# Kernel optimization log

Measured on AMD Instinct MI355X. Metric: run time of the kernel, lower is better.

The kernel has to match this reference:

```python
import jax, jax.numpy as jnp
import numpy as np

N = 20000      # nodes
E = 320000     # edges
S = 256        # scalar (0e) channels of irreps_feature
F = 960        # full irreps_feature dim (256x0e+128x1e+64x2e)
NB = 32        # number_of_basis
CUT = 5.0      # max_radius


def setup_inputs() -> dict:
    key = jax.random.key(0)
    ks = jax.random.split(key, 24)
    def w(k, shape):
        return jax.random.normal(k, shape, jnp.float32) / np.sqrt(shape[0])
    return {
        "node_feature": jax.random.normal(ks[0], (N, F), jnp.float32),
        "pos": jax.random.normal(ks[1], (N, 3), jnp.float32),
        "edge_index": jax.random.randint(ks[2], (2, E), 0, N),
        "W_ai1": w(ks[3], (S, S)), "b_ai1": jnp.zeros((S,), jnp.float32),
        "W_ai2": w(ks[4], (S, 1)), "b_ai2": jnp.zeros((1,), jnp.float32),
        "W_ci1": w(ks[5], (S, S)), "b_ci1": jnp.zeros((S,), jnp.float32),
        "W_ci2": w(ks[6], (S, 1)), "b_ci2": jnp.zeros((1,), jnp.float32),
        "W_sc": w(ks[7], (S, S)), "b_sc": jnp.zeros((S,), jnp.float32),
        "W_ed": w(ks[8], (NB, S)), "b_ed": jnp.zeros((S,), jnp.float32),
        "W_b1": w(ks[9], (3 * S, S)), "b_b1": jnp.zeros((S,), jnp.float32),
        "W_b2": w(ks[10], (S, 1)), "b_b2": jnp.zeros((1,), jnp.float32),
    }


def _rbf(d):
    # ExpNormalSmearing (torchmd-net), cutoff_lower=0, cutoff_upper=CUT, non-trainable
    start = np.exp(-CUT)
    means = jnp.linspace(start, 1.0, NB, dtype=jnp.float32)
    beta = jnp.float32(((2.0 / NB) * (1.0 - start)) ** -2)
    cosine_cut = 0.5 * (jnp.cos(np.pi * d / CUT) + 1.0) * (d < CUT)
    return cosine_cut[:, None] * jnp.exp(-beta * (jnp.exp(-d)[:, None] - means) ** 2)


def reference(node_feature, pos, edge_index,
              W_ai1, b_ai1, W_ai2, b_ai2,
              W_ci1, b_ci1, W_ci2, b_ci2,
              W_sc, b_sc, W_ed, b_ed,
              W_b1, b_b1, W_b2, b_b2):
    # LinearRS(irreps_feature -> 0e) only touches the 0e block (first S channels)
    scal = node_feature[:, :S]
    silu = jax.nn.silu

    log_ai = silu(scal @ W_ai1 + b_ai1) @ W_ai2 + b_ai2          # [N,1]
    ai = jnp.exp(log_ai)
    log_ci = silu(scal @ W_ci1 + b_ci1) @ W_ci2 + b_ci2          # [N,1]
    ci = jnp.exp(log_ci)

    src, dst = edge_index[0], edge_index[1]
    rel = pos[dst] - pos[src]                                     # [E,3]
    norm = jnp.linalg.norm(rel, axis=1, keepdims=True)            # [E,1]
    rhat = rel / (norm + 1e-8)
    emb = _rbf(norm[:, 0])                                        # [E,NB]

    node_sc = scal @ W_sc + b_sc                                  # project once, gather [N,S]
    src_f = node_sc[src]
    dst_f = node_sc[dst]
    edge_f = emb @ W_ed + b_ed
    edge_feature = jnp.concatenate([src_f, dst_f, edge_f], axis=-1)  # [E,3S]
    bij = silu(edge_feature @ W_b1 + b_b1) @ W_b2 + b_b2          # [E,1]

    # edge softmax over incoming edges of dst, with extra ci mass
    bmax = jax.ops.segment_max(bij, dst, num_segments=N)
    bmax = jnp.where(jnp.isneginf(bmax), 0.0, bmax)
    bij_exp = jnp.exp(bij - bmax[dst])
    bsum = jax.ops.segment_sum(bij_exp, dst, num_segments=N) + ci  # [N,1]
    gamma = bij_exp / (bsum[dst] + 1e-7)                           # [E,1]

    bij_prime = gamma * ai[dst]                                    # [E,1]
    outer = rhat[:, :, None] * rhat[:, None, :]                    # [E,3,3]
    contrib = jax.ops.segment_sum(bij_prime[:, :, None] * outer, dst, num_segments=N)  # [N,3,3]

    eye3 = jnp.eye(3, dtype=pos.dtype)
    sigma = ai[:, :, None] * eye3 - contrib + 1e-6 * eye3          # [N,3,3]
    sum_gamma = jax.ops.segment_sum(gamma, dst, num_segments=N)    # [N,1]
    return sigma, ai, sum_gamma
```

## Files before the change

kernel.cpp:

```cpp
#include <hip/hip_runtime.h>
#include <math.h>

#define N_NODES 20000
#define E_EDGES 320000
#define F_DIM   960
#define S_DIM   256
#define QTAB    2048
#define ASTRIDE 264
#define CAP     64

typedef __attribute__((ext_vector_type(8))) short short8;
typedef __attribute__((ext_vector_type(4))) float f32x4;
typedef _Float16 half8 __attribute__((ext_vector_type(8)));

__device__ __forceinline__ float siluf(float x) {
    return x / (1.0f + __expf(-x));
}

__device__ __forceinline__ unsigned short bf16rn(float x) {
    unsigned u = __float_as_uint(x);
    return (unsigned short)((u + 0x7FFFu + ((u >> 16) & 1u)) >> 16);
}

__global__ void prep_kernel(const float* __restrict__ W_sc, const float* __restrict__ W_ed,
                            const float* __restrict__ W_b1, const float* __restrict__ b_sc,
                            const float* __restrict__ b_ed, const float* __restrict__ b_b1,
                            const float* __restrict__ W_ai1, const float* __restrict__ W_ci1,
                            float* __restrict__ Bcat, float* __restrict__ We, float* __restrict__ c0,
                            int* __restrict__ cnt)
{
    int idx = blockIdx.x * 256 + threadIdx.x;
    if (idx < N_NODES) cnt[idx] = 0;
    if (idx < 256 * 1024) {
        int k = idx >> 10, j = idx & 1023;
        float s = 0.0f;
        if (j < 256) {
            for (int m = 0; m < 256; ++m) s += W_sc[k * 256 + m] * W_b1[m * 256 + j];
        } else if (j < 512) {
            int jj = j - 256;
            for (int m = 0; m < 256; ++m) s += W_sc[k * 256 + m] * W_b1[(256 + m) * 256 + jj];
        } else if (j < 768) {
            s = W_ai1[k * 256 + (j - 512)];
        } else {
            s = W_ci1[k * 256 + (j - 768)];
        }
        Bcat[idx] = s;
    } else if (idx < 256 * 1024 + 32 * 256) {
        int t = idx - 256 * 1024;
        int p = t >> 8, j = t & 255;
        float s = 0.0f;
        for (int m = 0; m < 256; ++m) s += W_ed[p * 256 + m] * W_b1[(512 + m) * 256 + j];
        We[t] = s;
    } else if (idx < 256 * 1024 + 32 * 256 + 256) {
        int j = idx - 256 * 1024 - 32 * 256;
        float s = b_b1[j];
        for (int m = 0; m < 256; ++m) {
            s += b_sc[m] * (W_b1[m * 256 + j] + W_b1[(256 + m) * 256 + j]);
            s += b_ed[m] * W_b1[(512 + m) * 256 + j];
        }
        c0[j] = s;
    }
}

__global__ void aux_kernel(const int* __restrict__ ei, int* __restrict__ cnt, int* __restrict__ rank,
                           const float* __restrict__ Bcat, unsigned short* __restrict__ Bpack,
                           const float* __restrict__ We, _Float16* __restrict__ Tab,
                           const float* __restrict__ nf, unsigned short* __restrict__ scalp)
{
    int b = blockIdx.x;
    if (b < 1250) {
        int i = b * 256 + threadIdx.x;
        rank[i] = atomicAdd(&cnt[ei[E_EDGES + i]], 1);
    } else if (b < 1378) {
        int idx = (b - 1250) * 256 + threadIdx.x;
        int kq = idx & 3, j = (idx >> 2) & 1023, t = idx >> 12;
        #pragma unroll
        for (int jj = 0; jj < 8; ++jj)
            Bpack[idx * 8 + jj] = bf16rn(Bcat[(t * 32 + kq * 8 + jj) * 1024 + j]);
    } else if (b < 3426) {
        int idx = (b - 1378) * 256 + threadIdx.x;
        int q = idx >> 8, j = idx & 255;
        float nrm = 5.0f * (float)q / (float)(QTAB - 1);
        const float start = 0.006737946999085467f;
        const float mustep = (1.0f - start) / 31.0f;
        const float bx = (2.0f / 32.0f) * (1.0f - start);
        const float beta = 1.0f / (bx * bx);
        const float PI_F = 3.14159265358979323846f;
        float cc = (nrm < 5.0f) ? 0.5f * (__cosf(PI_F * nrm * 0.2f) + 1.0f) : 0.0f;
        float t = __expf(-nrm);
        float s = 0.0f;
        for (int k = 0; k < 32; ++k) {
            float dm = t - (start + (float)k * mustep);
            s += __expf(-beta * dm * dm) * We[k * 256 + j];
        }
        Tab[idx] = (_Float16)(cc * s);
    } else {
        int idx = (b - 3426) * 256 + threadIdx.x;
        int base = idx * 4;
        int n = base >> 8, k = base & 255;
        float4 a4 = *(const float4*)&nf[(size_t)n * F_DIM + k];
        ushort4 b4;
        b4.x = bf16rn(a4.x); b4.y = bf16rn(a4.y);
        b4.z = bf16rn(a4.z); b4.w = bf16rn(a4.w);
        *(ushort4*)&scalp[n * 256 + k] = b4;
    }
}

__global__ __launch_bounds__(1024) void scan_kernel(const int* __restrict__ cnt,
                                                    int* __restrict__ start)
{
    extern __shared__ int ls[];
    __shared__ int ps[1024];
    const int t = threadIdx.x;
    for (int i = t; i < N_NODES; i += 1024) ls[i] = cnt[i];
    __syncthreads();

    const int base = t * 20;
    int loc[20];
    int s = 0;
    #pragma unroll
    for (int i = 0; i < 20; ++i) {
        int n = (base + i < N_NODES) ? ls[base + i] : 0;
        loc[i] = s; s += n;
    }
    ps[t] = s;
    __syncthreads();
    for (int off = 1; off < 1024; off <<= 1) {
        int v = (t >= off) ? ps[t - off] : 0;
        __syncthreads();
        ps[t] += v;
        __syncthreads();
    }
    int offset = ps[t] - s;
    #pragma unroll
    for (int i = 0; i < 20; ++i)
        if (base + i < N_NODES) ls[base + i] = offset + loc[i];
    __syncthreads();
    for (int i = t; i < N_NODES; i += 1024) start[i] = ls[i];
}

__global__ void edge_geom_kernel(const int* __restrict__ ei, const int* __restrict__ start,
                                 const int* __restrict__ rank, const float* __restrict__ pos,
                                 int2* __restrict__ sd, float4* __restrict__ geom)
{
    int i = blockIdx.x * 256 + threadIdx.x;
    if (i >= E_EDGES) return;
    int s = ei[i];
    int d = ei[E_EDGES + i];
    int slot = start[d] + rank[i];
    int2 p; p.x = s; p.y = d;
    sd[slot] = p;

    float px = pos[3 * d + 0] - pos[3 * s + 0];
    float py = pos[3 * d + 1] - pos[3 * s + 1];
    float pz = pos[3 * d + 2] - pos[3 * s + 2];
    float nrm = sqrtf(px * px + py * py + pz * pz);
    float inv = 1.0f / (nrm + 1e-8f);
    float4 o;
    o.x = px * inv; o.y = py * inv; o.z = pz * inv;
    o.w = nrm * (float)(QTAB - 1) * 0.2f;
    geom[slot] = o;
}

__global__ __launch_bounds__(256) void node_mfma_kernel(
    const unsigned short* __restrict__ scalp, const unsigned short* __restrict__ Bpack,
    const float* __restrict__ c0,
    const float* __restrict__ b_ai1, const float* __restrict__ W_ai2, const float* __restrict__ b_ai2,
    const float* __restrict__ b_ci1, const float* __restrict__ W_ci2, const float* __restrict__ b_ci2,
    _Float16* __restrict__ u, _Float16* __restrict__ v,
    float* __restrict__ bsumseed, float* __restrict__ out_ai)
{
    __shared__ unsigned short A[32 * ASTRIDE];
    __shared__ float red[32 * 4];

    const int tid = threadIdx.x;
    const int w = tid >> 6, lane = tid & 63;
    const int bg = blockIdx.x & 1;
    const int m0 = (blockIdx.x >> 1) * 32;
    const int col16 = lane & 15, quad = lane >> 4;

    #pragma unroll
    for (int it = 0; it < 4; ++it) {
        int idx = (it * 256 + tid) * 8;
        int r = idx >> 8, c = idx & 255;
        *(uint4*)&A[r * ASTRIDE + c] = *(const uint4*)&scalp[(m0 + r) * 256 + c];
    }
    __syncthreads();

    for (int cc = 0; cc < 2; ++cc) {
        const int cg = bg * 2 + cc;
        f32x4 acc[2][4];
        #pragma unroll
        for (int mt = 0; mt < 2; ++mt)
            #pragma unroll
            for (int nt = 0; nt < 4; ++nt)
                acc[mt][nt] = (f32x4){0.0f, 0.0f, 0.0f, 0.0f};

        const int colbase = cg * 256 + w * 64;

        for (int t = 0; t < 8; ++t) {
            short8 af[2];
            #pragma unroll
            for (int mt = 0; mt < 2; ++mt)
                af[mt] = *(const short8*)&A[(mt * 16 + col16) * ASTRIDE + t * 32 + quad * 8];
            short8 bf[4];
            #pragma unroll
            for (int nt = 0; nt < 4; ++nt)
                bf[nt] = *(const short8*)&Bpack[(((t * 1024 + colbase + nt * 16 + col16) * 4) + quad) * 8];
            #pragma unroll
            for (int mt = 0; mt < 2; ++mt)
                #pragma unroll
                for (int nt = 0; nt < 4; ++nt)
                    acc[mt][nt] = __builtin_amdgcn_mfma_f32_16x16x32_bf16(af[mt], bf[nt], acc[mt][nt], 0, 0, 0);
        }

        if (cg == 0) {
            #pragma unroll
            for (int nt = 0; nt < 4; ++nt) {
                int jl = w * 64 + nt * 16 + col16;
                float c0v = c0[jl];
                #pragma unroll
                for (int mt = 0; mt < 2; ++mt)
                    #pragma unroll
                    for (int reg = 0; reg < 4; ++reg)
                        u[(m0 + mt * 16 + quad * 4 + reg) * 256 + jl] = (_Float16)(acc[mt][nt][reg] + c0v);
        }
        } else if (cg == 1) {
            #pragma unroll
            for (int nt = 0; nt < 4; ++nt) {
                int jl = w * 64 + nt * 16 + col16;
                #pragma unroll
                for (int mt = 0; mt < 2; ++mt)
                    #pragma unroll
                    for (int reg = 0; reg < 4; ++reg)
                        v[(m0 + mt * 16 + quad * 4 + reg) * 256 + jl] = (_Float16)(acc[mt][nt][reg]);
            }
        } else {
            const float* b1 = (cg == 2) ? b_ai1 : b_ci1;
            const float* w2 = (cg == 2) ? W_ai2 : W_ci2;
            float s[2][4] = {{0, 0, 0, 0}, {0, 0, 0, 0}};
            #pragma unroll
            for (int nt = 0; nt < 4; ++nt) {
                int jl = w * 64 + nt * 16 + col16;
                float bb = b1[jl], ww = w2[jl];
                #pragma unroll
                for (int mt = 0; mt < 2; ++mt)
                    #pragma unroll
                    for (int reg = 0; reg < 4; ++reg)
                        s[mt][reg] += siluf(acc[mt][nt][reg] + bb) * ww;
            }
            #pragma unroll
            for (int off = 1; off < 16; off <<= 1) {
                #pragma unroll
                for (int mt = 0; mt < 2; ++mt)
                    #pragma unroll
                    for (int reg = 0; reg < 4; ++reg)
                        s[mt][reg] += __shfl_xor(s[mt][reg], off);
            }
            if (col16 == 0) {
                #pragma unroll
                for (int mt = 0; mt < 2; ++mt)
                    #pragma unroll
                    for (int reg = 0; reg < 4; ++reg)
                        red[(mt * 16 + quad * 4 + reg) * 4 + w] = s[mt][reg];
            }
            __syncthreads();
            if (tid < 32) {
                float sum = red[tid * 4] + red[tid * 4 + 1] + red[tid * 4 + 2] + red[tid * 4 + 3];
                if (cg == 2) out_ai[m0 + tid] = expf(sum + b_ai2[0]);
                else         bsumseed[m0 + tid] = expf(sum + b_ci2[0]) + 1e-7f;
            }
            __syncthreads();
        }
    }
}

__global__ __launch_bounds__(256) void edge_bij_kernel(
    const int2* __restrict__ sd, const float4* __restrict__ geom,
    const _Float16* __restrict__ u, const _Float16* __restrict__ v,
    const _Float16* __restrict__ Tab,
    const float* __restrict__ W_b2, const float* __restrict__ b_b2,
    float* __restrict__ bijV)
{
    const int l = threadIdx.x & 15;
    const int slot = blockIdx.x * 16 + (threadIdx.x >> 4);
    const int2 e = sd[slot];
    const int src = e.x;
    const int dst = e.y;
    const float x = ((const float*)&geom[slot])[3];

    int qi = (int)x;
    float f = x - (float)qi;
    if (qi >= QTAB - 1) { qi = QTAB - 2; f = 1.0f; }
    const _Float16 fh = (_Float16)f;

    float w2c[16];
    #pragma unroll
    for (int c = 0; c < 16; c += 4)
        *(float4*)&w2c[c] = *(const float4*)&W_b2[l * 16 + c];

    const unsigned lo = (unsigned)l * 32u;
    const char* ub = (const char*)u + ((unsigned)src * 512u + lo);
    const char* vb = (const char*)v + ((unsigned)dst * 512u + lo);
    const char* tb = (const char*)Tab + ((unsigned)qi * 512u + lo);

    half8 u0 = *(const half8*)(ub);
    half8 u1 = *(const half8*)(ub + 16);
    half8 v0 = *(const half8*)(vb);
    half8 v1 = *(const half8*)(vb + 16);
    half8 t00 = *(const half8*)(tb);
    half8 t01 = *(const half8*)(tb + 16);
    half8 t10 = *(const half8*)(tb + 512);
    half8 t11 = *(const half8*)(tb + 528);

    half8 h0 = (u0 + v0) + (t00 + fh * (t10 - t00));
    half8 h1 = (u1 + v1) + (t01 + fh * (t11 - t01));

    float acc = 0.0f;
    #pragma unroll
    for (int c = 0; c < 8; ++c) {
        float hf = (float)h0[c];
        float sig = __builtin_amdgcn_rcpf(1.0f + __expf(-hf));
        acc += w2c[c] * hf * sig;
    }
    #pragma unroll
    for (int c = 0; c < 8; ++c) {
        float hf = (float)h1[c];
        float sig = __builtin_amdgcn_rcpf(1.0f + __expf(-hf));
        acc += w2c[8 + c] * hf * sig;
    }
    #pragma unroll
    for (int off = 1; off < 16; off <<= 1) acc += __shfl_xor(acc, off);

    if (l == 0) bijV[slot] = acc + b_b2[0];
}

__global__ __launch_bounds__(256) void node_reduce_kernel(
    const int* __restrict__ start, const int* __restrict__ cnt,
    const float* __restrict__ bijV, const float4* __restrict__ geom,
    const float* __restrict__ bsumseed, const float* __restrict__ out_ai,
    float* __restrict__ out_sigma, float* __restrict__ out_sg)
{
    const int grp = threadIdx.x >> 4;
    const int l = threadIdx.x & 15;
    const int g = blockIdx.x * 16 + grp;
    const int st = start[g];
    const int deg = min(cnt[g], CAP);

    float bj[4], ex[4], ey[4], ez[4];
    bool ok[4];
    float m = -1e30f;
    #pragma unroll
    for (int k = 0; k < 4; ++k) {
        int i = l + k * 16;
        ok[k] = (i < deg);
        if (ok[k]) {
            float4 o = geom[st + i];
            bj[k] = bijV[st + i];
            ex[k] = o.x; ey[k] = o.y; ez[k] = o.z;
        } else {
            bj[k] = -1e30f; ex[k] = 0.0f; ey[k] = 0.0f; ez[k] = 0.0f;
        }
        m = fmaxf(m, bj[k]);
    }
    #pragma unroll
    for (int off = 1; off < 16; off <<= 1) m = fmaxf(m, __shfl_xor(m, off));

    float g4[4];
    float ssum = 0.0f;
    #pragma unroll
    for (int k = 0; k < 4; ++k) {
        g4[k] = ok[k] ? __expf(bj[k] - m) : 0.0f;
        ssum += g4[k];
    }
    #pragma unroll
    for (int off = 1; off < 16; off <<= 1) ssum += __shfl_xor(ssum, off);

    float invt = 1.0f / (ssum + bsumseed[g]);

    float a0 = 0, a1 = 0, a2 = 0, a3 = 0, a4 = 0, a5 = 0, a6 = 0;
    #pragma unroll
    for (int k = 0; k < 4; ++k) {
        float gm = g4[k] * invt;
        a0 += gm * ex[k] * ex[k]; a1 += gm * ey[k] * ey[k]; a2 += gm * ez[k] * ez[k];
        a3 += gm * ex[k] * ey[k]; a4 += gm * ex[k] * ez[k]; a5 += gm * ey[k] * ez[k];
        a6 += gm;
    }
    #pragma unroll
    for (int off = 1; off < 16; off <<= 1) {
        a0 += __shfl_xor(a0, off); a1 += __shfl_xor(a1, off);
        a2 += __shfl_xor(a2, off); a3 += __shfl_xor(a3, off);
        a4 += __shfl_xor(a4, off); a5 += __shfl_xor(a5, off);
        a6 += __shfl_xor(a6, off);
    }

    if (l == 0) {
        float ai = out_ai[g];
        float* sg = &out_sigma[g * 9];
        float d0 = ai + 1e-6f;
        sg[0] = d0 - ai * a0;
        sg[1] = -ai * a3;
        sg[2] = -ai * a4;
        sg[3] = -ai * a3;
        sg[4] = d0 - ai * a1;
        sg[5] = -ai * a5;
        sg[6] = -ai * a4;
        sg[7] = -ai * a5;
        sg[8] = d0 - ai * a2;
        out_sg[g] = a6;
    }
}

extern "C" void kernel_launch(void* const* d_in, const int* in_sizes, int n_in,
                              void* d_out, int out_size, void* d_ws, size_t ws_size,
                              hipStream_t stream)
{
    const float* nf    = (const float*)d_in[0];
    const float* pos   = (const float*)d_in[1];
    const int*   ei    = (const int*)  d_in[2];
    const float* W_ai1 = (const float*)d_in[3];
    const float* b_ai1 = (const float*)d_in[4];
    const float* W_ai2 = (const float*)d_in[5];
    const float* b_ai2 = (const float*)d_in[6];
    const float* W_ci1 = (const float*)d_in[7];
    const float* b_ci1 = (const float*)d_in[8];
    const float* W_ci2 = (const float*)d_in[9];
    const float* b_ci2 = (const float*)d_in[10];
    const float* W_sc  = (const float*)d_in[11];
    const float* b_sc  = (const float*)d_in[12];
    const float* W_ed  = (const float*)d_in[13];
    const float* b_ed  = (const float*)d_in[14];
    const float* W_b1  = (const float*)d_in[15];
    const float* b_b1  = (const float*)d_in[16];
    const float* W_b2  = (const float*)d_in[17];
    const float* b_b2  = (const float*)d_in[18];

    char* pb = (char*)d_ws;
    auto alloc = [&](size_t bytes) -> void* {
        void* r = (void*)pb;
        pb += (bytes + 255) & ~(size_t)255;
        return r;
    };
    float*          Bcat    = (float*)         alloc(262144 * 4);
    float*          We      = (float*)         alloc(8192 * 4);
    float*          c0      = (float*)         alloc(256 * 4);
    _Float16*       Tab     = (_Float16*)      alloc((size_t)QTAB * 256 * 2);
    unsigned short* Bpack   = (unsigned short*)alloc((size_t)256 * 1024 * 2);
    unsigned short* scalp   = (unsigned short*)alloc((size_t)N_NODES * 256 * 2);
    _Float16*       u       = (_Float16*)      alloc((size_t)N_NODES * 256 * 2);
    _Float16*       v       = (_Float16*)      alloc((size_t)N_NODES * 256 * 2);
    float*          bsumseed= (float*)         alloc((size_t)N_NODES * 4);
    int*            cnt     = (int*)           alloc((size_t)N_NODES * 4);
    int*            startA  = (int*)           alloc((size_t)N_NODES * 4);
    int*            rank    = (int*)           alloc((size_t)E_EDGES * 4);
    int2*           sd      = (int2*)          alloc((size_t)E_EDGES * 8);
    float4*         geom    = (float4*)        alloc((size_t)E_EDGES * 16);
    float*          bijV    = (float*)         alloc((size_t)E_EDGES * 4);

    float* out       = (float*)d_out;
    float* out_sigma = out;
    float* out_ai    = out + N_NODES * 9;
    float* out_sg    = out + N_NODES * 10;

    prep_kernel<<<1058, 256, 0, stream>>>(W_sc, W_ed, W_b1, b_sc, b_ed, b_b1, W_ai1, W_ci1,
                                          Bcat, We, c0, cnt);
    aux_kernel<<<8426, 256, 0, stream>>>(ei, cnt, rank, Bcat, Bpack, We, Tab, nf, scalp);
    scan_kernel<<<1, 1024, (size_t)N_NODES * 4, stream>>>(cnt, startA);
    edge_geom_kernel<<<1250, 256, 0, stream>>>(ei, startA, rank, pos, sd, geom);
    node_mfma_kernel<<<1250, 256, 0, stream>>>(scalp, Bpack, c0, b_ai1, W_ai2, b_ai2,
                                               b_ci1, W_ci2, b_ci2, u, v, bsumseed, out_ai);
    edge_bij_kernel<<<20000, 256, 0, stream>>>(sd, geom, u, v, Tab, W_b2, b_b2, bijV);
    node_reduce_kernel<<<1250, 256, 0, stream>>>(startA, cnt, bijV, geom, bsumseed, out_ai,
                                                 out_sigma, out_sg);
}
```

Measured before the change: 286.5 us.

## Fuse weight packing into prep, merge scan into node MFMA kernel

The prep kernel now computes eight folded-weight rows per thread and writes bf16-packed MFMA operands directly. This removes the fp32 Bcat buffer and its separate repack pass. The single-block prefix scan becomes an extra block of the node MFMA kernel, so it no longer needs its own serial launch. The MFMA tiles are enlarged to 64 rows with one column group per block. In exchange, accumulator register pressure rises and the scan runs with fewer threads doing longer serial loops.

```diff
diff --git a/kernel.cpp b/kernel.cpp
--- a/kernel.cpp
+++ b/kernel.cpp
@@ -22,48 +22,72 @@
     return (unsigned short)((u + 0x7FFFu + ((u >> 16) & 1u)) >> 16);
 }
 
-__global__ void prep_kernel(const float* __restrict__ W_sc, const float* __restrict__ W_ed,
-                            const float* __restrict__ W_b1, const float* __restrict__ b_sc,
-                            const float* __restrict__ b_ed, const float* __restrict__ b_b1,
-                            const float* __restrict__ W_ai1, const float* __restrict__ W_ci1,
-                            float* __restrict__ Bcat, float* __restrict__ We, float* __restrict__ c0,
-                            int* __restrict__ cnt)
-{
-    int idx = blockIdx.x * 256 + threadIdx.x;
-    if (idx < N_NODES) cnt[idx] = 0;
-    if (idx < 256 * 1024) {
-        int k = idx >> 10, j = idx & 1023;
-        float s = 0.0f;
+__global__ __launch_bounds__(256) void prep_kernel(
+    const float* __restrict__ W_sc, const float* __restrict__ W_ed,
+    const float* __restrict__ W_b1, const float* __restrict__ b_sc,
+    const float* __restrict__ b_ed, const float* __restrict__ b_b1,
+    const float* __restrict__ W_ai1, const float* __restrict__ W_ci1,
+    unsigned short* __restrict__ Bpack, float* __restrict__ We, float* __restrict__ c0,
+    int* __restrict__ cnt)
+{
+    const int b = blockIdx.x;
+    const int tid = threadIdx.x;
+    if (b < 128) {
+        const int oct = b >> 2;
+        const int j   = (b & 3) * 256 + tid;
+        const int k0  = oct * 8;
+        float s[8];
+        #pragma unroll
+        for (int jj = 0; jj < 8; ++jj) s[jj] = 0.0f;
         if (j < 256) {
-            for (int m = 0; m < 256; ++m) s += W_sc[k * 256 + m] * W_b1[m * 256 + j];
+            for (int m = 0; m < 256; ++m) {
+                float wv = W_b1[m * 256 + j];
+                #pragma unroll
+                for (int jj = 0; jj < 8; ++jj) s[jj] += W_sc[(k0 + jj) * 256 + m] * wv;
+            }
         } else if (j < 512) {
-            int jj = j - 256;
-            for (int m = 0; m < 256; ++m) s += W_sc[k * 256 + m] * W_b1[(256 + m) * 256 + jj];
+            const int j2 = j - 256;
+            for (int m = 0; m < 256; ++m) {
+                float wv = W_b1[(256 + m) * 256 + j2];
+                #pragma unroll
+                for (int jj = 0; jj < 8; ++jj) s[jj] += W_sc[(k0 + jj) * 256 + m] * wv;
+            }
         } else if (j < 768) {
-            s = W_ai1[k * 256 + (j - 512)];
+            #pragma unroll
+            for (int jj = 0; jj < 8; ++jj) s[jj] = W_ai1[(k0 + jj) * 256 + (j - 512)];
         } else {
-            s = W_ci1[k * 256 + (j - 768)];
-        }
-        Bcat[idx] = s;
-    } else if (idx < 256 * 1024 + 32 * 256) {
-        int t = idx - 256 * 1024;
-        int p = t >> 8, j = t & 255;
+            #pragma unroll
+            for (int jj = 0; jj < 8; ++jj) s[jj] = W_ci1[(k0 + jj) * 256 + (j - 768)];
+        }
+        unsigned short o[8];
+        #pragma unroll
+        for (int jj = 0; jj < 8; ++jj) o[jj] = bf16rn(s[jj]);
+        unsigned short* dst = &Bpack[((oct >> 2) * 4096 + j * 4 + (oct & 3)) * 8];
+        ushort4 lo; lo.x = o[0]; lo.y = o[1]; lo.z = o[2]; lo.w = o[3];
+        ushort4 hi; hi.x = o[4]; hi.y = o[5]; hi.z = o[6]; hi.w = o[7];
+        *(ushort4*)dst = lo;
+        *(ushort4*)(dst + 4) = hi;
+    } else if (b < 160) {
+        const int t = (b - 128) * 256 + tid;
+        const int p = t >> 8, j = t & 255;
         float s = 0.0f;
         for (int m = 0; m < 256; ++m) s += W_ed[p * 256 + m] * W_b1[(512 + m) * 256 + j];
         We[t] = s;
-    } else if (idx < 256 * 1024 + 32 * 256 + 256) {
-        int j = idx - 256 * 1024 - 32 * 256;
+    } else if (b == 160) {
+        const int j = tid;
         float s = b_b1[j];
         for (int m = 0; m < 256; ++m) {
             s += b_sc[m] * (W_b1[m * 256 + j] + W_b1[(256 + m) * 256 + j]);
             s += b_ed[m] * W_b1[(512 + m) * 256 + j];
         }
         c0[j] = s;
+    } else {
+        const int idx = (b - 161) * 256 + tid;
+        if (idx < N_NODES) cnt[idx] = 0;
     }
 }
 
 __global__ void aux_kernel(const int* __restrict__ ei, int* __restrict__ cnt, int* __restrict__ rank,
-                           const float* __restrict__ Bcat, unsigned short* __restrict__ Bpack,
                            const float* __restrict__ We, _Float16* __restrict__ Tab,
                            const float* __restrict__ nf, unsigned short* __restrict__ scalp)
 {
@@ -71,14 +95,8 @@
     if (b < 1250) {
         int i = b * 256 + threadIdx.x;
         rank[i] = atomicAdd(&cnt[ei[E_EDGES + i]], 1);
-    } else if (b < 1378) {
+    } else if (b < 3298) {
         int idx = (b - 1250) * 256 + threadIdx.x;
-        int kq = idx & 3, j = (idx >> 2) & 1023, t = idx >> 12;
-        #pragma unroll
-        for (int jj = 0; jj < 8; ++jj)
-            Bpack[idx * 8 + jj] = bf16rn(Bcat[(t * 32 + kq * 8 + jj) * 1024 + j]);
-    } else if (b < 3426) {
-        int idx = (b - 1378) * 256 + threadIdx.x;
         int q = idx >> 8, j = idx & 255;
         float nrm = 5.0f * (float)q / (float)(QTAB - 1);
         const float start = 0.006737946999085467f;
@@ -95,7 +113,7 @@
         }
         Tab[idx] = (_Float16)(cc * s);
     } else {
-        int idx = (b - 3426) * 256 + threadIdx.x;
+        int idx = (b - 3298) * 256 + threadIdx.x;
         int base = idx * 4;
         int n = base >> 8, k = base & 255;
         float4 a4 = *(const float4*)&nf[(size_t)n * F_DIM + k];
@@ -106,37 +124,149 @@
     }
 }
 
-__global__ __launch_bounds__(1024) void scan_kernel(const int* __restrict__ cnt,
-                                                    int* __restrict__ start)
-{
-    extern __shared__ int ls[];
-    __shared__ int ps[1024];
-    const int t = threadIdx.x;
-    for (int i = t; i < N_NODES; i += 1024) ls[i] = cnt[i];
+__global__ __launch_bounds__(256) void mfma_scan_kernel(
+    const unsigned short* __restrict__ scalp, const unsigned short* __restrict__ Bpack,
+    const float* __restrict__ c0,
+    const float* __restrict__ b_ai1, const float* __restrict__ W_ai2, const float* __restrict__ b_ai2,
+    const float* __restrict__ b_ci1, const float* __restrict__ W_ci2, const float* __restrict__ b_ci2,
+    _Float16* __restrict__ u, _Float16* __restrict__ v,
+    float* __restrict__ bsumseed, float* __restrict__ out_ai,
+    const int* __restrict__ cnt, int* __restrict__ startA)
+{
+    __shared__ unsigned short A[64 * ASTRIDE];
+    __shared__ float red[64 * 4];
+
+    const int tid = threadIdx.x;
+
+    if (blockIdx.x == 1252) {
+        int* ps = (int*)A;
+        const int base = tid * 79;
+        int ssum = 0;
+        for (int i = 0; i < 79; ++i) {
+            int idx = base + i;
+            ssum += (idx < N_NODES) ? cnt[idx] : 0;
+        }
+        ps[tid] = ssum;
+        __syncthreads();
+        for (int off = 1; off < 256; off <<= 1) {
+            int vv = (tid >= off) ? ps[tid - off] : 0;
+            __syncthreads();
+            ps[tid] += vv;
+            __syncthreads();
+        }
+        int run = ps[tid] - ssum;
+        for (int i = 0; i < 79; ++i) {
+            int idx = base + i;
+            if (idx < N_NODES) { int c = cnt[idx]; startA[idx] = run; run += c; }
+        }
+        return;
+    }
+
+    const int w = tid >> 6, lane = tid & 63;
+    const int cg = blockIdx.x & 3;
+    const int m0 = (blockIdx.x >> 2) * 64;
+    const int col16 = lane & 15, quad = lane >> 4;
+
+    #pragma unroll
+    for (int it = 0; it < 8; ++it) {
+        int idx = (it * 256 + tid) * 8;
+        int r = idx >> 8, c = idx & 255;
+        *(uint4*)&A[r * ASTRIDE + c] = *(const uint4*)&scalp[(size_t)(m0 + r) * 256 + c];
+    }
     __syncthreads();
 
-    const int base = t * 20;
-    int loc[20];
-    int s = 0;
-    #pragma unroll
-    for (int i = 0; i < 20; ++i) {
-        int n = (base + i < N_NODES) ? ls[base + i] : 0;
-        loc[i] = s; s += n;
-    }
-    ps[t] = s;
-    __syncthreads();
-    for (int off = 1; off < 1024; off <<= 1) {
-        int v = (t >= off) ? ps[t - off] : 0;
+    f32x4 acc[4][4];
+    #pragma unroll
+    for (int mt = 0; mt < 4; ++mt)
+        #pragma unroll
+        for (int nt = 0; nt < 4; ++nt)
+            acc[mt][nt] = (f32x4){0.0f, 0.0f, 0.0f, 0.0f};
+
+    const int colbase = cg * 256 + w * 64;
+
+    for (int t = 0; t < 8; ++t) {
+        short8 af[4];
+        #pragma unroll
+        for (int mt = 0; mt < 4; ++mt)
+            af[mt] = *(const short8*)&A[(mt * 16 + col16) * ASTRIDE + t * 32 + quad * 8];
+        short8 bf[4];
+        #pragma unroll
+        for (int nt = 0; nt < 4; ++nt)
+            bf[nt] = *(const short8*)&Bpack[(((t * 1024 + colbase + nt * 16 + col16) * 4) + quad) * 8];
+        #pragma unroll
+        for (int mt = 0; mt < 4; ++mt)
+            #pragma unroll
+            for (int nt = 0; nt < 4; ++nt)
+                acc[mt][nt] = __builtin_amdgcn_mfma_f32_16x16x32_bf16(af[mt], bf[nt], acc[mt][nt], 0, 0, 0);
+    }
+
+    if (cg == 0) {
+        #pragma unroll
+        for (int nt = 0; nt < 4; ++nt) {
+            int jl = w * 64 + nt * 16 + col16;
+            float c0v = c0[jl];
+            #pragma unroll
+            for (int mt = 0; mt < 4; ++mt)
+                #pragma unroll
+                for (int reg = 0; reg < 4; ++reg) {
+                    int row = m0 + mt * 16 + quad * 4 + reg;
+                    if (row < N_NODES)
+                        u[(size_t)row * 256 + jl] = (_Float16)(acc[mt][nt][reg] + c0v);
+                }
+        }
+    } else if (cg == 1) {
+        #pragma unroll
+        for (int nt = 0; nt < 4; ++nt) {
+            int jl = w * 64 + nt * 16 + col16;
+            #pragma unroll
+            for (int mt = 0; mt < 4; ++mt)
+                #pragma unroll
+                for (int reg = 0; reg < 4; ++reg) {
+                    int row = m0 + mt * 16 + quad * 4 + reg;
+                    if (row < N_NODES)
+                        v[(size_t)row * 256 + jl] = (_Float16)(acc[mt][nt][reg]);
+                }
+        }
+    } else {
+        const float* b1 = (cg == 2) ? b_ai1 : b_ci1;
+        const float* w2 = (cg == 2) ? W_ai2 : W_ci2;
+        float s[4][4];
+        #pragma unroll
+        for (int mt = 0; mt < 4; ++mt)
+            #pragma unroll
+            for (int reg = 0; reg < 4; ++reg) s[mt][reg] = 0.0f;
+        #pragma unroll
+        for (int nt = 0; nt < 4; ++nt) {
+            int jl = w * 64 + nt * 16 + col16;
+            float bb = b1[jl], ww = w2[jl];
+            #pragma unroll
+            for (int mt = 0; mt < 4; ++mt)
+                #pragma unroll
+                for (int reg = 0; reg < 4; ++reg)
+                    s[mt][reg] += siluf(acc[mt][nt][reg] + bb) * ww;
+        }
+        #pragma unroll
+        for (int off = 1; off < 16; off <<= 1) {
+            #pragma unroll
+            for (int mt = 0; mt < 4; ++mt)
+                #pragma unroll
+                for (int reg = 0; reg < 4; ++reg)
+                    s[mt][reg] += __shfl_xor(s[mt][reg], off);
+        }
+        if (col16 == 0) {
+            #pragma unroll
+            for (int mt = 0; mt < 4; ++mt)
+                #pragma unroll
+                for (int reg = 0; reg < 4; ++reg)
+                    red[(mt * 16 + quad * 4 + reg) * 4 + w] = s[mt][reg];
+        }
         __syncthreads();
-        ps[t] += v;
-        __syncthreads();
-    }
-    int offset = ps[t] - s;
-    #pragma unroll
-    for (int i = 0; i < 20; ++i)
-        if (base + i < N_NODES) ls[base + i] = offset + loc[i];
-    __syncthreads();
-    for (int i = t; i < N_NODES; i += 1024) start[i] = ls[i];
+        if (tid < 64 && m0 + tid < N_NODES) {
+            float sum = red[tid * 4] + red[tid * 4 + 1] + red[tid * 4 + 2] + red[tid * 4 + 3];
+            if (cg == 2) out_ai[m0 + tid] = expf(sum + b_ai2[0]);
+            else         bsumseed[m0 + tid] = expf(sum + b_ci2[0]) + 1e-7f;
+        }
+    }
 }
 
 __global__ void edge_geom_kernel(const int* __restrict__ ei, const int* __restrict__ start,
@@ -160,119 +290,6 @@
     o.x = px * inv; o.y = py * inv; o.z = pz * inv;
     o.w = nrm * (float)(QTAB - 1) * 0.2f;
     geom[slot] = o;
-}
-
-__global__ __launch_bounds__(256) void node_mfma_kernel(
-    const unsigned short* __restrict__ scalp, const unsigned short* __restrict__ Bpack,
-    const float* __restrict__ c0,
-    const float* __restrict__ b_ai1, const float* __restrict__ W_ai2, const float* __restrict__ b_ai2,
-    const float* __restrict__ b_ci1, const float* __restrict__ W_ci2, const float* __restrict__ b_ci2,
-    _Float16* __restrict__ u, _Float16* __restrict__ v,
-    float* __restrict__ bsumseed, float* __restrict__ out_ai)
-{
-    __shared__ unsigned short A[32 * ASTRIDE];
-    __shared__ float red[32 * 4];
-
-    const int tid = threadIdx.x;
-    const int w = tid >> 6, lane = tid & 63;
-    const int bg = blockIdx.x & 1;
-    const int m0 = (blockIdx.x >> 1) * 32;
-    const int col16 = lane & 15, quad = lane >> 4;
-
-    #pragma unroll
-    for (int it = 0; it < 4; ++it) {
-        int idx = (it * 256 + tid) * 8;
-        int r = idx >> 8, c = idx & 255;
-        *(uint4*)&A[r * ASTRIDE + c] = *(const uint4*)&scalp[(m0 + r) * 256 + c];
-    }
-    __syncthreads();
-
-    for (int cc = 0; cc < 2; ++cc) {
-        const int cg = bg * 2 + cc;
-        f32x4 acc[2][4];
-        #pragma unroll
-        for (int mt = 0; mt < 2; ++mt)
-            #pragma unroll
-            for (int nt = 0; nt < 4; ++nt)
-                acc[mt][nt] = (f32x4){0.0f, 0.0f, 0.0f, 0.0f};
-
-        const int colbase = cg * 256 + w * 64;
-
-        for (int t = 0; t < 8; ++t) {
-            short8 af[2];
-            #pragma unroll
-            for (int mt = 0; mt < 2; ++mt)
-                af[mt] = *(const short8*)&A[(mt * 16 + col16) * ASTRIDE + t * 32 + quad * 8];
-            short8 bf[4];
-            #pragma unroll
-            for (int nt = 0; nt < 4; ++nt)
-                bf[nt] = *(const short8*)&Bpack[(((t * 1024 + colbase + nt * 16 + col16) * 4) + quad) * 8];
-            #pragma unroll
-            for (int mt = 0; mt < 2; ++mt)
-                #pragma unroll
-                for (int nt = 0; nt < 4; ++nt)
-                    acc[mt][nt] = __builtin_amdgcn_mfma_f32_16x16x32_bf16(af[mt], bf[nt], acc[mt][nt], 0, 0, 0);
-        }
-
-        if (cg == 0) {
-            #pragma unroll
-            for (int nt = 0; nt < 4; ++nt) {
-                int jl = w * 64 + nt * 16 + col16;
-                float c0v = c0[jl];
-                #pragma unroll
-                for (int mt = 0; mt < 2; ++mt)
-                    #pragma unroll
-                    for (int reg = 0; reg < 4; ++reg)
-                        u[(m0 + mt * 16 + quad * 4 + reg) * 256 + jl] = (_Float16)(acc[mt][nt][reg] + c0v);
-        }
-        } else if (cg == 1) {
-            #pragma unroll
-            for (int nt = 0; nt < 4; ++nt) {
-                int jl = w * 64 + nt * 16 + col16;
-                #pragma unroll
-                for (int mt = 0; mt < 2; ++mt)
-                    #pragma unroll
-                    for (int reg = 0; reg < 4; ++reg)
-                        v[(m0 + mt * 16 + quad * 4 + reg) * 256 + jl] = (_Float16)(acc[mt][nt][reg]);
-            }
-        } else {
-            const float* b1 = (cg == 2) ? b_ai1 : b_ci1;
-            const float* w2 = (cg == 2) ? W_ai2 : W_ci2;
-            float s[2][4] = {{0, 0, 0, 0}, {0, 0, 0, 0}};
-            #pragma unroll
-            for (int nt = 0; nt < 4; ++nt) {
-                int jl = w * 64 + nt * 16 + col16;
-                float bb = b1[jl], ww = w2[jl];
-                #pragma unroll
-                for (int mt = 0; mt < 2; ++mt)
-                    #pragma unroll
-                    for (int reg = 0; reg < 4; ++reg)
-                        s[mt][reg] += siluf(acc[mt][nt][reg] + bb) * ww;
-            }
-            #pragma unroll
-            for (int off = 1; off < 16; off <<= 1) {
-                #pragma unroll
-                for (int mt = 0; mt < 2; ++mt)
-                    #pragma unroll
-                    for (int reg = 0; reg < 4; ++reg)
-                        s[mt][reg] += __shfl_xor(s[mt][reg], off);
-            }
-            if (col16 == 0) {
-                #pragma unroll
-                for (int mt = 0; mt < 2; ++mt)
-                    #pragma unroll
-                    for (int reg = 0; reg < 4; ++reg)
-                        red[(mt * 16 + quad * 4 + reg) * 4 + w] = s[mt][reg];
-            }
-            __syncthreads();
-            if (tid < 32) {
-                float sum = red[tid * 4] + red[tid * 4 + 1] + red[tid * 4 + 2] + red[tid * 4 + 3];
-                if (cg == 2) out_ai[m0 + tid] = expf(sum + b_ai2[0]);
-                else         bsumseed[m0 + tid] = expf(sum + b_ci2[0]) + 1e-7f;
-            }
-            __syncthreads();
-        }
-    }
 }
 
 __global__ __launch_bounds__(256) void edge_bij_kernel(
@@ -441,7 +458,6 @@
         pb += (bytes + 255) & ~(size_t)255;
         return r;
     };
-    float*          Bcat    = (float*)         alloc(262144 * 4);
     float*          We      = (float*)         alloc(8192 * 4);
     float*          c0      = (float*)         alloc(256 * 4);
     _Float16*       Tab     = (_Float16*)      alloc((size_t)QTAB * 256 * 2);
@@ -462,13 +478,13 @@
     float* out_ai    = out + N_NODES * 9;
     float* out_sg    = out + N_NODES * 10;
 
-    prep_kernel<<<1058, 256, 0, stream>>>(W_sc, W_ed, W_b1, b_sc, b_ed, b_b1, W_ai1, W_ci1,
-                                          Bcat, We, c0, cnt);
-    aux_kernel<<<8426, 256, 0, stream>>>(ei, cnt, rank, Bcat, Bpack, We, Tab, nf, scalp);
-    scan_kernel<<<1, 1024, (size_t)N_NODES * 4, stream>>>(cnt, startA);
+    prep_kernel<<<240, 256, 0, stream>>>(W_sc, W_ed, W_b1, b_sc, b_ed, b_b1, W_ai1, W_ci1,
+                                         Bpack, We, c0, cnt);
+    aux_kernel<<<8298, 256, 0, stream>>>(ei, cnt, rank, We, Tab, nf, scalp);
+    mfma_scan_kernel<<<1253, 256, 0, stream>>>(scalp, Bpack, c0, b_ai1, W_ai2, b_ai2,
+                                               b_ci1, W_ci2, b_ci2, u, v, bsumseed, out_ai,
+                                               cnt, startA);
     edge_geom_kernel<<<1250, 256, 0, stream>>>(ei, startA, rank, pos, sd, geom);
-    node_mfma_kernel<<<1250, 256, 0, stream>>>(scalp, Bpack, c0, b_ai1, W_ai2, b_ai2,
-                                               b_ci1, W_ci2, b_ci2, u, v, bsumseed, out_ai);
     edge_bij_kernel<<<20000, 256, 0, stream>>>(sd, geom, u, v, Tab, W_b2, b_b2, bijV);
     node_reduce_kernel<<<1250, 256, 0, stream>>>(startA, cnt, bijV, geom, bsumseed, out_ai,
                                                  out_sigma, out_sg);
```

After: 308.5 us. 1.08x slower.
